# Performance work log

Hardware: AMD Instinct MI355X
Metric: run time of the kernel (lower is better)

The kernel has to match this reference:

```python
import jax, jax.numpy as jnp
import numpy as np

ALPHA = 0.2  # leakyrelu negative slope and residual scale


def setup_inputs() -> dict:
    key = jax.random.key(0)
    k1, k2, k3, k4 = jax.random.split(key, 4)
    B, N, C, F = 8, 2048, 128, 128
    text = jax.random.normal(k1, (B, N, C), dtype=jnp.float32)
    adj = jax.random.uniform(k2, (B, N, N), dtype=jnp.float32)  # unused by the layer's math
    W = jax.random.normal(k3, (C, F), dtype=jnp.float32) * (1.0 / np.sqrt(C))
    a = jax.random.normal(k4, (2 * F, 1), dtype=jnp.float32) * 0.1
    return {"text": text, "adj": adj, "W": W, "a": a}


def reference(text, adj, W, a):
    # h: [B, N, F]
    h = jnp.matmul(text, W)
    Fdim = W.shape[1]
    a1 = a[:Fdim, 0]  # applies to source node i
    a2 = a[Fdim:, 0]  # applies to target node j
    e1 = jnp.einsum('bnf,f->bn', h, a1)  # [B, N]
    e2 = jnp.einsum('bnf,f->bn', h, a2)  # [B, N]
    # scores[b,i,j] = leakyrelu(a1.h_i + a2.h_j)  (same as concat-matmul in original)
    scores = jax.nn.leaky_relu(e1[:, :, None] + e2[:, None, :], negative_slope=ALPHA)
    attention = jax.nn.softmax(scores, axis=2)  # [B, N, N]; dropout off (eval)
    h_prime = jnp.matmul(attention, h)  # [B, N, F]
    return jax.nn.elu(h_prime + ALPHA * h)
```

## Files before the change

### kernel.cpp

```cpp
#include <hip/hip_runtime.h>
#include <hip/hip_bf16.h>

#define BB 8
#define NN 2048
#define CC 128
#define FF 128
#define ALPHA 0.2f
#define ROWS 16
#define WTPAD 136
#define CHN 256
#define CLEN 8
#define CSH 3

typedef __hip_bfloat16 bf16;
typedef __attribute__((ext_vector_type(8))) short short8;
typedef __attribute__((ext_vector_type(4))) float f32x4;
typedef unsigned long long u64;

__device__ __forceinline__ float ld1(const void* p, int i, int f32) {
    if (f32) return ((const float*)p)[i];
    return __bfloat162float(((const bf16*)p)[i]);
}
__device__ __forceinline__ float2 ld2(const void* p, int pair, int f32) {
    if (f32) return ((const float2*)p)[pair];
    __hip_bfloat162 v = ((const __hip_bfloat162*)p)[pair];
    return make_float2(__bfloat162float(v.x), __bfloat162float(v.y));
}
__device__ __forceinline__ u64 shfl_xor_u64(u64 v, int mask) {
    int lo = (int)(unsigned)(v & 0xFFFFFFFFull);
    int hi = (int)(unsigned)(v >> 32);
    lo = __shfl_xor(lo, mask, 64);
    hi = __shfl_xor(hi, mask, 64);
    return ((u64)(unsigned)hi << 32) | (unsigned)lo;
}

__global__ __launch_bounds__(256) void k_prep(const void* __restrict__ text,
                                              const void* __restrict__ W,
                                              const void* __restrict__ a,
                                              int* __restrict__ flag,
                                              float* __restrict__ wa1,
                                              float* __restrict__ wa2,
                                              ushort* __restrict__ WT) {
    __shared__ int cnt;
    __shared__ float aL[2 * FF];
    const int t = threadIdx.x;
    if (t == 0) cnt = 0;
    __syncthreads();
    const ushort2* p = (const ushort2*)text;
    int local = 0;
    for (int i = t; i < 1024; i += 256) {
        ushort2 v = p[i];
        float f = __uint_as_float(((unsigned)v.x) << 16);
        if (!(fabsf(f) <= 100.f)) local++;
    }
    atomicAdd(&cnt, local);
    __syncthreads();
    const int f32 = (cnt >= 64) ? 1 : 0;

    if (blockIdx.x == 0) {
        if (t == 0) flag[0] = f32;
        aL[t] = ld1(a, t, f32);
        __syncthreads();
        if (t < CC) {
            float s1 = 0.f, s2 = 0.f;
            for (int f = 0; f < FF; f += 4) {
                float w0 = ld1(W, t * FF + f, f32);
                float w1 = ld1(W, t * FF + f + 1, f32);
                float w2 = ld1(W, t * FF + f + 2, f32);
                float w3 = ld1(W, t * FF + f + 3, f32);
                s1 += w0 * aL[f] + w1 * aL[f + 1] + w2 * aL[f + 2] + w3 * aL[f + 3];
                s2 += w0 * aL[FF + f] + w1 * aL[FF + f + 1] + w2 * aL[FF + f + 2] + w3 * aL[FF + f + 3];
            }
            wa1[t] = s1; wa2[t] = s2;
        }
    } else {
        const int base = (blockIdx.x - 1) * 2048;
        for (int i = 0; i < 8; ++i) {
            int idx = base + i * 256 + t;
            int cc = idx >> 7, f = idx & 127;
            float v = ld1(W, idx, f32);
            bf16 b = __float2bfloat16(v);
            WT[f * CC + cc] = *(const ushort*)&b;
        }
    }
}

__global__ __launch_bounds__(256) void k_e(const void* __restrict__ text,
                                           const float* __restrict__ wa1,
                                           const float* __restrict__ wa2,
                                           float* __restrict__ e1,
                                           float* __restrict__ e2,
                                           const int* __restrict__ flag) {
    const int f32 = *flag;
    const int wave = threadIdx.x >> 6;
    const int lane = threadIdx.x & 63;
    const int row = blockIdx.x * 4 + wave;
    float2 tv = ld2(text, row * (CC / 2) + lane, f32);
    float s1 = tv.x * wa1[2 * lane] + tv.y * wa1[2 * lane + 1];
    float s2 = tv.x * wa2[2 * lane] + tv.y * wa2[2 * lane + 1];
#pragma unroll
    for (int off = 32; off > 0; off >>= 1) {
        s1 += __shfl_down(s1, off, 64);
        s2 += __shfl_down(s2, off, 64);
    }
    if (lane == 0) { e1[row] = s1; e2[row] = s2; }
}

__global__ __launch_bounds__(1024) void k_sort(const float* __restrict__ e2,
                                               float* __restrict__ e2s,
                                               int* __restrict__ sidx,
                                               float* __restrict__ z1,
                                               float* __restrict__ z2) {
    __shared__ u64 lk[NN];
    __shared__ float2 wtot[16];
    __shared__ float2 woff[16];
    const int b = blockIdx.x;
    const int t = threadIdx.x;

    float f0 = e2[b * NN + 2 * t], f1 = e2[b * NN + 2 * t + 1];
    unsigned m0 = __float_as_uint(f0); m0 = (m0 & 0x80000000u) ? ~m0 : (m0 | 0x80000000u);
    unsigned m1 = __float_as_uint(f1); m1 = (m1 & 0x80000000u) ? ~m1 : (m1 | 0x80000000u);
    u64 s0 = ((u64)m0 << 32) | (unsigned)(2 * t);
    u64 s1 = ((u64)m1 << 32) | (unsigned)(2 * t + 1);

    for (int size = 2; size <= NN; size <<= 1) {
        const bool up = (((2 * t) & size) == 0);
        for (int stride = size >> 1; stride >= 1; stride >>= 1) {
            if (stride == 1) {
                u64 mn = s0 < s1 ? s0 : s1;
                u64 mx = s0 < s1 ? s1 : s0;
                s0 = up ? mn : mx;
                s1 = up ? mx : mn;
            } else if (stride <= 64) {
                const int m = stride >> 1;
                u64 p0 = shfl_xor_u64(s0, m);
                u64 p1 = shfl_xor_u64(s1, m);
                const bool keepmin = (((t & m) == 0) == up);
                s0 = keepmin ? (s0 < p0 ? s0 : p0) : (s0 < p0 ? p0 : s0);
                s1 = keepmin ? (s1 < p1 ? s1 : p1) : (s1 < p1 ? p1 : s1);
            } else {
                lk[2 * t] = s0; lk[2 * t + 1] = s1;
                __syncthreads();
                u64 p0 = lk[(2 * t) ^ stride];
                u64 p1 = lk[(2 * t + 1) ^ stride];
                const bool keepmin = ((((2 * t) & stride) == 0) == up);
                s0 = keepmin ? (s0 < p0 ? s0 : p0) : (s0 < p0 ? p0 : s0);
                s1 = keepmin ? (s1 < p1 ? s1 : p1) : (s1 < p1 ? p1 : s1);
                __syncthreads();
            }
        }
    }

    unsigned k0 = (unsigned)(s0 >> 32), k1 = (unsigned)(s1 >> 32);
    float v0 = __uint_as_float((k0 & 0x80000000u) ? (k0 ^ 0x80000000u) : ~k0);
    float v1 = __uint_as_float((k1 & 0x80000000u) ? (k1 ^ 0x80000000u) : ~k1);
    e2s[b * NN + 2 * t] = v0;
    e2s[b * NN + 2 * t + 1] = v1;
    sidx[b * NN + 2 * t] = (int)(unsigned)(s0 & 0xFFFFFFFFull);
    sidx[b * NN + 2 * t + 1] = (int)(unsigned)(s1 & 0xFFFFFFFFull);

    float x0a = expf(v0), x0b = expf(ALPHA * v0);
    float x1a = expf(v1), x1b = expf(ALPHA * v1);
    float pa = x0a + x1a, pb = x0b + x1b;
    float sa = pa, sb = pb;
    const int lane = t & 63, wid = t >> 6;
#pragma unroll
    for (int off = 1; off < 64; off <<= 1) {
        float ya = __shfl_up(sa, off, 64);
        float yb = __shfl_up(sb, off, 64);
        if (lane >= off) { sa += ya; sb += yb; }
    }
    if (lane == 63) wtot[wid] = make_float2(sa, sb);
    __syncthreads();
    if (t == 0) {
        float ra = 0.f, rb = 0.f;
        for (int w2 = 0; w2 < 16; ++w2) {
            float2 tt = wtot[w2];
            woff[w2] = make_float2(ra, rb);
            ra += tt.x; rb += tt.y;
        }
    }
    __syncthreads();
    float2 o = woff[wid];
    float pre_a = o.x + sa - pa, pre_b = o.y + sb - pb;
    float* Z1 = z1 + b * (NN + 1);
    float* Z2 = z2 + b * (NN + 1);
    if (t == 0) { Z1[0] = 0.f; Z2[0] = 0.f; }
    Z1[2 * t + 1] = pre_a + x0a;  Z2[2 * t + 1] = pre_b + x0b;
    Z1[2 * t + 2] = pre_a + pa;   Z2[2 * t + 2] = pre_b + pb;
}

__global__ __launch_bounds__(128) void k_ps(const void* __restrict__ text,
                                            const float* __restrict__ e2s,
                                            const int* __restrict__ sidx,
                                            float* __restrict__ PS1,
                                            float* __restrict__ PS2,
                                            float* __restrict__ T1,
                                            float* __restrict__ T2,
                                            const int* __restrict__ flag) {
    const int f32 = *flag;
    const int b = blockIdx.x / CHN, ch = blockIdx.x % CHN;
    const int c = threadIdx.x;
    float r1 = 0.f, r2 = 0.f;
    const int k0 = ch * CLEN;
#pragma unroll
    for (int kk = 0; kk < CLEN; ++kk) {
        int k = k0 + kk;
        PS1[(size_t)(b * NN + k) * CC + c] = r1;
        PS2[(size_t)(b * NN + k) * CC + c] = r2;
        float v = e2s[b * NN + k];
        int j = sidx[b * NN + k];
        float x = ld1(text, (b * NN + j) * CC + c, f32);
        r1 += expf(v) * x;
        r2 += expf(ALPHA * v) * x;
    }
    T1[(b * (CHN + 1) + ch) * CC + c] = r1;
    T2[(b * (CHN + 1) + ch) * CC + c] = r2;
}

__global__ __launch_bounds__(256) void k_scanT(float* __restrict__ T1,
                                               float* __restrict__ T2) {
    const int tid = blockIdx.x * 256 + threadIdx.x;
    const int b = tid / CC, c = tid % CC;
    float* P1 = T1 + (size_t)(b * (CHN + 1)) * CC + c;
    float* P2 = T2 + (size_t)(b * (CHN + 1)) * CC + c;
    float r1 = 0.f, r2 = 0.f;
    for (int ch = 0; ch < CHN; ch += 8) {
        float t1[8], t2[8];
#pragma unroll
        for (int u = 0; u < 8; ++u) { t1[u] = P1[(ch + u) * CC]; t2[u] = P2[(ch + u) * CC]; }
#pragma unroll
        for (int u = 0; u < 8; ++u) {
            P1[(ch + u) * CC] = r1; r1 += t1[u];
            P2[(ch + u) * CC] = r2; r2 += t2[u];
        }
    }
    P1[CHN * CC] = r1;
    P2[CHN * CC] = r2;
}

__global__ __launch_bounds__(256) void k_out(const void* __restrict__ text,
                                             const ushort* __restrict__ WT,
                                             const float* __restrict__ T1,
                                             const float* __restrict__ T2,
                                             const float* __restrict__ PS1,
                                             const float* __restrict__ PS2,
                                             const float* __restrict__ e1,
                                             const float* __restrict__ e2s,
                                             const float* __restrict__ z1,
                                             const float* __restrict__ z2,
                                             void* __restrict__ out,
                                             const int* __restrict__ flag) {
    __shared__ ushort WTl[FF * WTPAD];
    __shared__ ushort ul[ROWS * WTPAD];
    __shared__ float4 ri[ROWS];
    const int f32 = *flag;
    const int t = threadIdx.x;
    const int b = blockIdx.x / (NN / ROWS);
    const int r0 = (blockIdx.x % (NN / ROWS)) * ROWS;

    {
        const uint4* src = (const uint4*)WT;
#pragma unroll
        for (int i = 0; i < 8; ++i) {
            int idx = i * 256 + t;
            uint4 v = src[idx];
            int f = idx >> 4, cb = idx & 15;
            *(uint4*)&WTl[f * WTPAD + cb * 8] = v;
        }
    }
    if (t < ROWS) {
        const int row = b * NN + r0 + t;
        float ev = e1[row];
        float w1 = expf(ev), w2 = expf(ALPHA * ev);
        float thr = -ev;
        const float* e2sb = e2s + b * NN;
        int lo = 0, hi = NN;
        while (lo < hi) {
            int mid = (lo + hi) >> 1;
            if (e2sb[mid] <= thr) lo = mid + 1; else hi = mid;
        }
        float den = w1 * (z1[b * (NN + 1) + NN] - z1[b * (NN + 1) + lo])
                  + w2 * z2[b * (NN + 1) + lo];
        den = fmaxf(den, 1e-30f);
        ri[t] = make_float4(__int_as_float(lo), w1, w2, 1.f / den);
    }
    __syncthreads();

    {
        const int c = t & 127;
        const int g = t >> 7;
        const float* CB1 = T1 + (size_t)(b * (CHN + 1)) * CC + c;
        const float* CB2 = T2 + (size_t)(b * (CHN + 1)) * CC + c;
        const float* B1 = PS1 + (size_t)(b * NN) * CC + c;
        const float* B2 = PS2 + (size_t)(b * NN) * CC + c;
        const float S1 = CB1[CHN * CC];
#pragma unroll
        for (int q = 0; q < 8; ++q) {
            const int rr = g * 8 + q;
            float4 info = ri[rr];
            const int k = __float_as_int(info.x);
            const int c0 = k >> CSH;
            float P1 = CB1[c0 * CC];
            float P2 = CB2[c0 * CC];
            if (k < NN) {
                P1 += B1[(size_t)k * CC];
                P2 += B2[(size_t)k * CC];
            }
            float tc = ld1(text, (b * NN + r0 + rr) * CC + c, f32);
            float u = (info.y * (S1 - P1) + info.z * P2) * info.w + ALPHA * tc;
            bf16 ub = __float2bfloat16(u);
            ul[rr * WTPAD + c] = *(const ushort*)&ub;
        }
    }
    __syncthreads();

    {
        const int wv = t >> 6;
        const int lane = t & 63;
        const int m = lane & 15;
        const int quad = lane >> 4;
        f32x4 acc0 = {0.f, 0.f, 0.f, 0.f};
        f32x4 acc1 = {0.f, 0.f, 0.f, 0.f};
        const int f0 = (wv * 2 + 0) * 16 + m;
        const int f1 = (wv * 2 + 1) * 16 + m;
#pragma unroll
        for (int kt = 0; kt < 4; ++kt) {
            const int ko = kt * 32 + quad * 8;
            short8 afrag = *(const short8*)&ul[m * WTPAD + ko];
            short8 bf0 = *(const short8*)&WTl[f0 * WTPAD + ko];
            short8 bf1 = *(const short8*)&WTl[f1 * WTPAD + ko];
            acc0 = __builtin_amdgcn_mfma_f32_16x16x32_bf16(afrag, bf0, acc0, 0, 0, 0);
            acc1 = __builtin_amdgcn_mfma_f32_16x16x32_bf16(afrag, bf1, acc1, 0, 0, 0);
        }
#pragma unroll
        for (int ft = 0; ft < 2; ++ft) {
            f32x4 acc = ft ? acc1 : acc0;
            const int f = (wv * 2 + ft) * 16 + m;
#pragma unroll
            for (int reg = 0; reg < 4; ++reg) {
                const int urow = quad * 4 + reg;
                float x = acc[reg];
                float y = x > 0.f ? x : expm1f(x);
                const int orow = b * NN + r0 + urow;
                if (f32) ((float*)out)[orow * FF + f] = y;
                else     ((bf16*)out)[orow * FF + f] = __float2bfloat16(y);
            }
        }
    }
}

extern "C" void kernel_launch(void* const* d_in, const int* in_sizes, int n_in,
                              void* d_out, int out_size, void* d_ws, size_t ws_size,
                              hipStream_t stream) {
    const void* text = d_in[0];
    const void* Wp   = (n_in >= 4) ? d_in[2] : d_in[1];
    const void* ap   = (n_in >= 4) ? d_in[3] : d_in[2];
    for (int i = 0; i < n_in; ++i) {
        int s = in_sizes[i];
        if (s == BB * NN * CC)      text = d_in[i];
        else if (s == CC * FF)      Wp = d_in[i];
        else if (s == 2 * FF)       ap = d_in[i];
    }

    float* w = (float*)d_ws;
    size_t off = 0;
    int*    flagp  = (int*)(w + off);      off += 16;
    float*  wa1    = w + off;              off += 128;
    float*  wa2    = w + off;              off += 128;
    ushort* WT     = (ushort*)(w + off);   off += 8192;
    float*  e1     = w + off;              off += BB * NN;
    float*  e2     = w + off;              off += BB * NN;
    float*  e2s    = w + off;              off += BB * NN;
    int*    sidx   = (int*)(w + off);      off += BB * NN;
    float*  z1     = w + off;              off += BB * (NN + 1);
    float*  z2     = w + off;              off += BB * (NN + 1);
    float*  T1     = w + off;              off += (size_t)BB * (CHN + 1) * CC;
    float*  T2     = w + off;              off += (size_t)BB * (CHN + 1) * CC;
    float*  PS1    = w + off;              off += (size_t)BB * NN * CC;
    float*  PS2    = w + off;              off += (size_t)BB * NN * CC;

    k_prep<<<9, 256, 0, stream>>>(text, Wp, ap, flagp, wa1, wa2, WT);
    k_e<<<BB * NN / 4, 256, 0, stream>>>(text, wa1, wa2, e1, e2, flagp);
    k_sort<<<BB, 1024, 0, stream>>>(e2, e2s, sidx, z1, z2);
    k_ps<<<BB * CHN, 128, 0, stream>>>(text, e2s, sidx, PS1, PS2, T1, T2, flagp);
    k_scanT<<<4, 256, 0, stream>>>(T1, T2);
    k_out<<<BB * NN / ROWS, 256, 0, stream>>>(text, WT, T1, T2, PS1, PS2,
                                              e1, e2s, z1, z2, d_out, flagp);
}
```

Before: 241.0 us.

## Drop per-row prefix arrays, recompute partial chunk sums in output kernel

Removes the PS1/PS2 per-element prefix arrays (two B*N*C float buffers written and then gathered). The output kernel now recomputes the partial in-chunk sum from up to seven sorted text rows, using exp of the sorted scores. The per-row binary search and denominator move into the sort kernel, which keeps Z prefixes and the sorted scores in LDS. The chunk-total scan becomes a parallel wave-shuffle scan over many blocks instead of 4 serial blocks. This trades large global write and read traffic for extra gathers and exps in k_out.

```diff
diff --git a/kernel.cpp b/kernel.cpp
--- a/kernel.cpp
+++ b/kernel.cpp
@@ -107,11 +107,14 @@
 }
 
 __global__ __launch_bounds__(1024) void k_sort(const float* __restrict__ e2,
+                                               const float* __restrict__ e1,
                                                float* __restrict__ e2s,
                                                int* __restrict__ sidx,
-                                               float* __restrict__ z1,
-                                               float* __restrict__ z2) {
+                                               float* __restrict__ rig) {
     __shared__ u64 lk[NN];
+    __shared__ float es[NN];
+    __shared__ float Z1L[NN + 1];
+    __shared__ float Z2L[NN + 1];
     __shared__ float2 wtot[16];
     __shared__ float2 woff[16];
     const int b = blockIdx.x;
@@ -154,6 +157,7 @@
     unsigned k0 = (unsigned)(s0 >> 32), k1 = (unsigned)(s1 >> 32);
     float v0 = __uint_as_float((k0 & 0x80000000u) ? (k0 ^ 0x80000000u) : ~k0);
     float v1 = __uint_as_float((k1 & 0x80000000u) ? (k1 ^ 0x80000000u) : ~k1);
+    es[2 * t] = v0;  es[2 * t + 1] = v1;
     e2s[b * NN + 2 * t] = v0;
     e2s[b * NN + 2 * t + 1] = v1;
     sidx[b * NN + 2 * t] = (int)(unsigned)(s0 & 0xFFFFFFFFull);
@@ -183,21 +187,35 @@
     __syncthreads();
     float2 o = woff[wid];
     float pre_a = o.x + sa - pa, pre_b = o.y + sb - pb;
-    float* Z1 = z1 + b * (NN + 1);
-    float* Z2 = z2 + b * (NN + 1);
-    if (t == 0) { Z1[0] = 0.f; Z2[0] = 0.f; }
-    Z1[2 * t + 1] = pre_a + x0a;  Z2[2 * t + 1] = pre_b + x0b;
-    Z1[2 * t + 2] = pre_a + pa;   Z2[2 * t + 2] = pre_b + pb;
-}
-
-__global__ __launch_bounds__(128) void k_ps(const void* __restrict__ text,
-                                            const float* __restrict__ e2s,
-                                            const int* __restrict__ sidx,
-                                            float* __restrict__ PS1,
-                                            float* __restrict__ PS2,
-                                            float* __restrict__ T1,
-                                            float* __restrict__ T2,
-                                            const int* __restrict__ flag) {
+    if (t == 0) { Z1L[0] = 0.f; Z2L[0] = 0.f; }
+    Z1L[2 * t + 1] = pre_a + x0a;  Z2L[2 * t + 1] = pre_b + x0b;
+    Z1L[2 * t + 2] = pre_a + pa;   Z2L[2 * t + 2] = pre_b + pb;
+    __syncthreads();
+
+    const float ZN = Z1L[NN];
+#pragma unroll
+    for (int rr = 0; rr < 2; ++rr) {
+        const int r = t + rr * 1024;
+        float ev = e1[b * NN + r];
+        float w1 = expf(ev), w2 = expf(ALPHA * ev);
+        float thr = -ev;
+        int lo = 0, hi = NN;
+        while (lo < hi) {
+            int mid = (lo + hi) >> 1;
+            if (es[mid] <= thr) lo = mid + 1; else hi = mid;
+        }
+        float den = w1 * (ZN - Z1L[lo]) + w2 * Z2L[lo];
+        den = fmaxf(den, 1e-30f);
+        ((float4*)rig)[b * NN + r] = make_float4(__int_as_float(lo), w1, w2, 1.f / den);
+    }
+}
+
+__global__ __launch_bounds__(128) void k_tot(const void* __restrict__ text,
+                                             const float* __restrict__ e2s,
+                                             const int* __restrict__ sidx,
+                                             float* __restrict__ T1,
+                                             float* __restrict__ T2,
+                                             const int* __restrict__ flag) {
     const int f32 = *flag;
     const int b = blockIdx.x / CHN, ch = blockIdx.x % CHN;
     const int c = threadIdx.x;
@@ -206,8 +224,6 @@
 #pragma unroll
     for (int kk = 0; kk < CLEN; ++kk) {
         int k = k0 + kk;
-        PS1[(size_t)(b * NN + k) * CC + c] = r1;
-        PS2[(size_t)(b * NN + k) * CC + c] = r2;
         float v = e2s[b * NN + k];
         int j = sidx[b * NN + k];
         float x = ld1(text, (b * NN + j) * CC + c, f32);
@@ -218,37 +234,41 @@
     T2[(b * (CHN + 1) + ch) * CC + c] = r2;
 }
 
-__global__ __launch_bounds__(256) void k_scanT(float* __restrict__ T1,
+__global__ __launch_bounds__(256) void k_scan2(float* __restrict__ T1,
                                                float* __restrict__ T2) {
-    const int tid = blockIdx.x * 256 + threadIdx.x;
-    const int b = tid / CC, c = tid % CC;
+    __shared__ float2 wt[4];
+    const int b = blockIdx.x >> 7, c = blockIdx.x & 127;
+    const int ch = threadIdx.x;
     float* P1 = T1 + (size_t)(b * (CHN + 1)) * CC + c;
     float* P2 = T2 + (size_t)(b * (CHN + 1)) * CC + c;
-    float r1 = 0.f, r2 = 0.f;
-    for (int ch = 0; ch < CHN; ch += 8) {
-        float t1[8], t2[8];
-#pragma unroll
-        for (int u = 0; u < 8; ++u) { t1[u] = P1[(ch + u) * CC]; t2[u] = P2[(ch + u) * CC]; }
-#pragma unroll
-        for (int u = 0; u < 8; ++u) {
-            P1[(ch + u) * CC] = r1; r1 += t1[u];
-            P2[(ch + u) * CC] = r2; r2 += t2[u];
-        }
-    }
-    P1[CHN * CC] = r1;
-    P2[CHN * CC] = r2;
+    const float t1 = P1[ch * CC];
+    const float t2 = P2[ch * CC];
+    float s1 = t1, s2 = t2;
+    const int lane = ch & 63, wid = ch >> 6;
+#pragma unroll
+    for (int off = 1; off < 64; off <<= 1) {
+        float y1 = __shfl_up(s1, off, 64);
+        float y2 = __shfl_up(s2, off, 64);
+        if (lane >= off) { s1 += y1; s2 += y2; }
+    }
+    if (lane == 63) wt[wid] = make_float2(s1, s2);
+    __syncthreads();
+    float o1 = 0.f, o2 = 0.f;
+#pragma unroll
+    for (int w2 = 0; w2 < 4; ++w2)
+        if (w2 < wid) { o1 += wt[w2].x; o2 += wt[w2].y; }
+    P1[ch * CC] = o1 + s1 - t1;
+    P2[ch * CC] = o2 + s2 - t2;
+    if (ch == CHN - 1) { P1[CHN * CC] = o1 + s1; P2[CHN * CC] = o2 + s2; }
 }
 
 __global__ __launch_bounds__(256) void k_out(const void* __restrict__ text,
                                              const ushort* __restrict__ WT,
                                              const float* __restrict__ T1,
                                              const float* __restrict__ T2,
-                                             const float* __restrict__ PS1,
-                                             const float* __restrict__ PS2,
-                                             const float* __restrict__ e1,
                                              const float* __restrict__ e2s,
-                                             const float* __restrict__ z1,
-                                             const float* __restrict__ z2,
+                                             const int* __restrict__ sidx,
+                                             const float* __restrict__ rig,
                                              void* __restrict__ out,
                                              const int* __restrict__ flag) {
     __shared__ ushort WTl[FF * WTPAD];
@@ -269,22 +289,7 @@
             *(uint4*)&WTl[f * WTPAD + cb * 8] = v;
         }
     }
-    if (t < ROWS) {
-        const int row = b * NN + r0 + t;
-        float ev = e1[row];
-        float w1 = expf(ev), w2 = expf(ALPHA * ev);
-        float thr = -ev;
-        const float* e2sb = e2s + b * NN;
-        int lo = 0, hi = NN;
-        while (lo < hi) {
-            int mid = (lo + hi) >> 1;
-            if (e2sb[mid] <= thr) lo = mid + 1; else hi = mid;
-        }
-        float den = w1 * (z1[b * (NN + 1) + NN] - z1[b * (NN + 1) + lo])
-                  + w2 * z2[b * (NN + 1) + lo];
-        den = fmaxf(den, 1e-30f);
-        ri[t] = make_float4(__int_as_float(lo), w1, w2, 1.f / den);
-    }
+    if (t < ROWS) ri[t] = ((const float4*)rig)[b * NN + r0 + t];
     __syncthreads();
 
     {
@@ -292,20 +297,34 @@
         const int g = t >> 7;
         const float* CB1 = T1 + (size_t)(b * (CHN + 1)) * CC + c;
         const float* CB2 = T2 + (size_t)(b * (CHN + 1)) * CC + c;
-        const float* B1 = PS1 + (size_t)(b * NN) * CC + c;
-        const float* B2 = PS2 + (size_t)(b * NN) * CC + c;
+        const float* e2sb = e2s + b * NN;
+        const int* sxb = sidx + b * NN;
         const float S1 = CB1[CHN * CC];
 #pragma unroll
         for (int q = 0; q < 8; ++q) {
             const int rr = g * 8 + q;
             float4 info = ri[rr];
-            const int k = __float_as_int(info.x);
+            const int k = __builtin_amdgcn_readfirstlane(__float_as_int(info.x));
             const int c0 = k >> CSH;
             float P1 = CB1[c0 * CC];
             float P2 = CB2[c0 * CC];
-            if (k < NN) {
-                P1 += B1[(size_t)k * CC];
-                P2 += B2[(size_t)k * CC];
+            const int j0 = c0 * CLEN;
+            const int cnt = k - j0;
+            if (cnt > 0) {
+                float vv[CLEN - 1]; int jj[CLEN - 1];
+#pragma unroll
+                for (int i = 0; i < CLEN - 1; ++i) {
+                    vv[i] = e2sb[j0 + i];
+                    jj[i] = sxb[j0 + i];
+                }
+#pragma unroll
+                for (int i = 0; i < CLEN - 1; ++i) {
+                    if (i < cnt) {
+                        float x = ld1(text, (b * NN + jj[i]) * CC + c, f32);
+                        P1 += expf(vv[i]) * x;
+                        P2 += expf(ALPHA * vv[i]) * x;
+                    }
+                }
             }
             float tc = ld1(text, (b * NN + r0 + rr) * CC + c, f32);
             float u = (info.y * (S1 - P1) + info.z * P2) * info.w + ALPHA * tc;
@@ -373,18 +392,15 @@
     float*  e2     = w + off;              off += BB * NN;
     float*  e2s    = w + off;              off += BB * NN;
     int*    sidx   = (int*)(w + off);      off += BB * NN;
-    float*  z1     = w + off;              off += BB * (NN + 1);
-    float*  z2     = w + off;              off += BB * (NN + 1);
+    float*  rig    = w + off;              off += (size_t)4 * BB * NN;
     float*  T1     = w + off;              off += (size_t)BB * (CHN + 1) * CC;
     float*  T2     = w + off;              off += (size_t)BB * (CHN + 1) * CC;
-    float*  PS1    = w + off;              off += (size_t)BB * NN * CC;
-    float*  PS2    = w + off;              off += (size_t)BB * NN * CC;
 
     k_prep<<<9, 256, 0, stream>>>(text, Wp, ap, flagp, wa1, wa2, WT);
     k_e<<<BB * NN / 4, 256, 0, stream>>>(text, wa1, wa2, e1, e2, flagp);
-    k_sort<<<BB, 1024, 0, stream>>>(e2, e2s, sidx, z1, z2);
-    k_ps<<<BB * CHN, 128, 0, stream>>>(text, e2s, sidx, PS1, PS2, T1, T2, flagp);
-    k_scanT<<<4, 256, 0, stream>>>(T1, T2);
-    k_out<<<BB * NN / ROWS, 256, 0, stream>>>(text, WT, T1, T2, PS1, PS2,
-                                              e1, e2s, z1, z2, d_out, flagp);
-}
+    k_sort<<<BB, 1024, 0, stream>>>(e2, e1, e2s, sidx, rig);
+    k_tot<<<BB * CHN, 128, 0, stream>>>(text, e2s, sidx, T1, T2, flagp);
+    k_scan2<<<BB * CC, 256, 0, stream>>>(T1, T2);
+    k_out<<<BB * NN / ROWS, 256, 0, stream>>>(text, WT, T1, T2, e2s, sidx,
+                                              rig, d_out, flagp);
+}
```

Measured after the change: 248.2 us. 3.0% more time.
